# Kernel optimization log

Measured on AMD Instinct MI355X. Metric: run time of the kernel, lower is better.

## Reference

```python
import jax, jax.numpy as jnp
import numpy as np

N_EMBD = 512
Q_N_EMBD = 512
N_HEAD = 8
EPS = 1e-5


def _layernorm(x, w, b):
    mu = jnp.mean(x, axis=-1, keepdims=True)
    var = jnp.mean(jnp.square(x - mu), axis=-1, keepdims=True)
    return (x - mu) * jax.lax.rsqrt(var + EPS) * w + b


def setup_inputs() -> dict:
    key = jax.random.key(0)
    ks = jax.random.split(key, 16)
    B, C, H, W = 8, N_EMBD, 32, 32
    s = 1.0 / np.sqrt(N_EMBD)
    inp = {
        "q": jax.random.normal(ks[0], (B, Q_N_EMBD, H, W), jnp.float32),
        "kv": jax.random.normal(ks[1], (B, C, H, W), jnp.float32),
        "ln_kv_w": jnp.ones((N_EMBD,), jnp.float32),
        "ln_kv_b": jnp.zeros((N_EMBD,), jnp.float32),
        "ln_q_w": jnp.ones((Q_N_EMBD,), jnp.float32),
        "ln_q_b": jnp.zeros((Q_N_EMBD,), jnp.float32),
        "Wk": jax.random.normal(ks[2], (N_EMBD, N_EMBD), jnp.float32) * s,
        "bk": jnp.zeros((N_EMBD,), jnp.float32),
        "Wq": jax.random.normal(ks[3], (Q_N_EMBD, N_EMBD), jnp.float32) * s,
        "bq": jnp.zeros((N_EMBD,), jnp.float32),
        "Wv": jax.random.normal(ks[4], (N_EMBD, N_EMBD), jnp.float32) * s,
        "bv": jnp.zeros((N_EMBD,), jnp.float32),
        "Wp": jax.random.normal(ks[5], (N_EMBD, N_EMBD), jnp.float32) * s,
        "bp": jnp.zeros((N_EMBD,), jnp.float32),
    }
    return inp


def reference(q, kv, ln_kv_w, ln_kv_b, ln_q_w, ln_q_b,
              Wk, bk, Wq, bq, Wv, bv, Wp, bp):
    B, C, H, W = kv.shape
    c_q = q.shape[1]
    T = H * W
    hd = C // N_HEAD  # head dim

    # [B, C, H, W] -> [B, T, C] tokens
    kv_t = kv.reshape(B, C, T).transpose(0, 2, 1)
    q_t = q.reshape(B, c_q, T).transpose(0, 2, 1)

    kv_n = _layernorm(kv_t, ln_kv_w, ln_kv_b)
    q_n = _layernorm(q_t, ln_q_w, ln_q_b)

    # projections, split heads: [B, T, C] -> [B, H, T, hd]
    def heads(x):
        return x.reshape(B, T, N_HEAD, hd).transpose(0, 2, 1, 3)

    k = heads(kv_n @ Wk + bk)
    qh = heads(q_n @ Wq + bq)
    v = heads(kv_n @ Wv + bv)

    att = jnp.einsum('bhqd,bhkd->bhqk', qh, k) * (1.0 / np.sqrt(hd))
    att = jax.nn.softmax(att, axis=-1)
    y = jnp.einsum('bhqk,bhkd->bhqd', att, v)
    y = y.transpose(0, 2, 1, 3).reshape(B, T, C)
    y = y @ Wp + bp

    x = kv_t + y  # residual on (pre-LN) kv tokens
    return x.transpose(0, 2, 1).reshape(B, C, H, W)
```

## Files before the change

### kernel.cpp

```cpp
#include <hip/hip_runtime.h>
#include <stdint.h>

#define DI static __device__ __forceinline__

typedef __attribute__((ext_vector_type(8))) short bh8;
typedef __attribute__((ext_vector_type(4))) float f4;
typedef __attribute__((ext_vector_type(4))) unsigned int u4;

DI short f2bf(float f) {
  unsigned u = __float_as_uint(f);
  u += 0x7fffu + ((u >> 16) & 1u);
  return (short)(u >> 16);
}

DI unsigned pkbf(float a, float b) {
  unsigned ua = __float_as_uint(a) + 0x8000u;
  unsigned ub = __float_as_uint(b) + 0x8000u;
  return __builtin_amdgcn_perm(ub, ua, 0x07060302u);
}

DI void gll16(const void* g, void* l) {
  __builtin_amdgcn_global_load_lds(
      (const __attribute__((address_space(1))) unsigned int*)g,
      (__attribute__((address_space(3))) unsigned int*)l, 16, 0, 0);
}

DI f4 mfma16(bh8 a, bh8 b, f4 c) {
  return __builtin_amdgcn_mfma_f32_16x16x32_bf16(a, b, c, 0, 0, 0);
}

DI bh8 ld8(const short* p) { return *(const bh8*)p; }

__global__ __launch_bounds__(256) void prep_k(
    const float* __restrict__ kv, const float* __restrict__ qi,
    const float* __restrict__ kw, const float* __restrict__ kbv,
    const float* __restrict__ qw, const float* __restrict__ qbv,
    const float* __restrict__ Wk, const float* __restrict__ Wq,
    const float* __restrict__ Wv, const float* __restrict__ Wp,
    short* __restrict__ kvn, short* __restrict__ qn,
    short* __restrict__ Wt)
{
  __shared__ char sm[16 * 516 * 4 + 128];
  int role = blockIdx.y;
  int bx = blockIdx.x;
  int tid = threadIdx.x;

  if (role < 4) {
    if (bx >= 256) return;
    float (*ts)[33] = (float(*)[33])sm;
    const float* w = (role == 0) ? Wk : (role == 1) ? Wq : (role == 2) ? Wv : Wp;
    short* o = Wt + ((size_t)role << 18);
    int c0 = (bx & 15) << 5, r0 = (bx >> 4) << 5;
    int tx = tid & 31, ty = tid >> 5;
#pragma unroll
    for (int k = 0; k < 32; k += 8)
      ts[ty + k][tx] = w[((size_t)(r0 + ty + k) << 9) + c0 + tx];
    __syncthreads();
#pragma unroll
    for (int k = 0; k < 32; k += 8)
      o[((size_t)(c0 + ty + k) << 9) + r0 + tx] = f2bf(ts[tx][ty + k]);
    return;
  }

  float (*xs)[516] = (float(*)[516])sm;
  float* smean = (float*)(sm + 16 * 516 * 4);
  float* srstd = smean + 16;
  int which = role - 4;
  const float* x = which ? qi : kv;
  const float* w = which ? qw : kw;
  const float* bb = which ? qbv : kbv;
  short* o = which ? qn : kvn;
  int b = bx >> 6;
  int t0 = (bx & 63) << 4;
  const float* xb = x + ((size_t)b << 19) + (size_t)t0;
#pragma unroll
  for (int k = 0; k < 8; k++) {
    int idx = (k << 8) + tid;
    int c = idx >> 2, tt = (idx & 3) << 2;
    float4 v = *(const float4*)(xb + ((size_t)c << 10) + tt);
    xs[tt + 0][c] = v.x; xs[tt + 1][c] = v.y;
    xs[tt + 2][c] = v.z; xs[tt + 3][c] = v.w;
  }
  __syncthreads();
  {
    int t = tid >> 4, cp = tid & 15;
    float s = 0.f, s2 = 0.f;
#pragma unroll
    for (int k = 0; k < 8; k++) {
      float4 v = *(const float4*)&xs[t][(cp << 2) + (k << 6)];
      s  += v.x + v.y + v.z + v.w;
      s2 += v.x * v.x + v.y * v.y + v.z * v.z + v.w * v.w;
    }
#pragma unroll
    for (int m = 1; m < 16; m <<= 1) {
      s  += __shfl_xor(s,  m);
      s2 += __shfl_xor(s2, m);
    }
    if (cp == 0) {
      float mean = s * (1.f / 512.f);
      float var  = s2 * (1.f / 512.f) - mean * mean;
      smean[t] = mean;
      srstd[t] = rsqrtf(var + 1e-5f);
    }
  }
  __syncthreads();
#pragma unroll
  for (int k = 0; k < 8; k++) {
    int idx = (k << 8) + tid;
    int t = idx >> 7, c = (idx & 127) << 2;
    float4 v = *(const float4*)&xs[t][c];
    float4 wv = *(const float4*)(w + c);
    float4 bv4 = *(const float4*)(bb + c);
    float mu = smean[t], rs = srstd[t];
    float r0 = (v.x - mu) * rs * wv.x + bv4.x;
    float r1 = (v.y - mu) * rs * wv.y + bv4.y;
    float r2 = (v.z - mu) * rs * wv.z + bv4.z;
    float r3 = (v.w - mu) * rs * wv.w + bv4.w;
    uint2 pk; pk.x = pkbf(r0, r1); pk.y = pkbf(r2, r3);
    *(uint2*)(o + (((size_t)(b << 10) + t0 + t) << 9) + c) = pk;
  }
}

__global__ __launch_bounds__(256) void gemm_qkv_k(
    const short* __restrict__ kvn, const short* __restrict__ qn,
    const short* __restrict__ Wt,
    const float* __restrict__ bk, const float* __restrict__ bq,
    const float* __restrict__ bv,
    short* __restrict__ kbuf, short* __restrict__ qbuf,
    short* __restrict__ vtb)
{
  __shared__ short As[128 * 32];
  __shared__ short Bs[128 * 32];
  int z = blockIdx.z;
  const short* A; const short* Bt; const float* bias; short* outp;
  int m0, n0;
  if (z == 0)      { A = kvn;            Bt = Wt;             bias = bk; outp = kbuf; }
  else if (z == 1) { A = qn;             Bt = Wt + (1 << 18); bias = bq; outp = qbuf; }
  else             { A = Wt + (2 << 18); Bt = kvn;            bias = bv; outp = vtb; }
  if (z == 2) { m0 = blockIdx.y << 7; n0 = blockIdx.x << 7; }
  else        { m0 = blockIdx.x << 7; n0 = blockIdx.y << 7; }
  int tid = threadIdx.x;
  int lane = tid & 63, wid = tid >> 6;
  int r = lane & 15, g = lane >> 4;
  int wrow = (wid >> 1) << 6, wcol = (wid & 1) << 6;
  f4 acc[4][4];
#pragma unroll
  for (int i = 0; i < 4; i++)
#pragma unroll
    for (int j = 0; j < 4; j++) {
      acc[i][j][0] = 0.f; acc[i][j][1] = 0.f;
      acc[i][j][2] = 0.f; acc[i][j][3] = 0.f;
    }
  const short* Ag = A  + ((size_t)(m0 + (tid >> 2)) << 9) + ((tid & 3) << 3);
  const short* Bg = Bt + ((size_t)(n0 + (tid >> 2)) << 9) + ((tid & 3) << 3);
  short* Asl = As + tid * 8;
  short* Bsl = Bs + tid * 8;
  for (int k0 = 0; k0 < 512; k0 += 32) {
    __syncthreads();
    gll16(Ag + k0,            Asl);
    gll16(Ag + k0 + 64 * 512, Asl + 2048);
    gll16(Bg + k0,            Bsl);
    gll16(Bg + k0 + 64 * 512, Bsl + 2048);
    __syncthreads();
    bh8 a[4], b[4];
#pragma unroll
    for (int i = 0; i < 4; i++)
      a[i] = ld8(As + ((wrow + (i << 4) + r) << 5) + (g << 3));
#pragma unroll
    for (int j = 0; j < 4; j++)
      b[j] = ld8(Bs + ((wcol + (j << 4) + r) << 5) + (g << 3));
#pragma unroll
    for (int i = 0; i < 4; i++)
#pragma unroll
      for (int j = 0; j < 4; j++)
        acc[i][j] = mfma16(a[i], b[j], acc[i][j]);
  }
#pragma unroll
  for (int i = 0; i < 4; i++) {
#pragma unroll
    for (int j = 0; j < 4; j++) {
      int mm = m0 + wrow + (i << 4) + (g << 2);
      int nn = n0 + wcol + (j << 4) + r;
      if (z != 2) {
        float bvv = bias[nn];
        int h = nn >> 6, d = nn & 63;
#pragma unroll
        for (int q = 0; q < 4; q++) {
          int m = mm + q;
          int bb = m >> 10, t = m & 1023;
          outp[((((size_t)(bb * 8 + h)) << 10) + t) * 64 + d] =
              f2bf(acc[i][j][q] + bvv);
        }
      } else {
        int bb = nn >> 10, t = nn & 1023;
#pragma unroll
        for (int q = 0; q < 4; q++) {
          int m = mm + q;
          int h = m >> 6, d = m & 63;
          outp[((((size_t)(bb * 8 + h)) << 6) + d) * 1024 + t] =
              f2bf(acc[i][j][q] + bias[m]);
        }
      }
    }
  }
}

__global__ __launch_bounds__(256) void gemm_proj_k(
    const short* __restrict__ A, const short* __restrict__ Bt,
    const float* __restrict__ bias, float* __restrict__ outp,
    const float* __restrict__ resid)
{
  __shared__ short As[64 * 32];
  __shared__ short Bs[128 * 32];
  int m0 = blockIdx.y << 6, n0 = blockIdx.x << 7;
  int tid = threadIdx.x;
  int lane = tid & 63, wid = tid >> 6;
  int r = lane & 15, g = lane >> 4;
  int wrow = (wid >> 1) << 5, wcol = (wid & 1) << 6;
  f4 acc[2][4];
#pragma unroll
  for (int i = 0; i < 2; i++)
#pragma unroll
    for (int j = 0; j < 4; j++) {
      acc[i][j][0] = 0.f; acc[i][j][1] = 0.f;
      acc[i][j][2] = 0.f; acc[i][j][3] = 0.f;
    }
  const short* Ag = A  + ((size_t)(m0 + (tid >> 2)) << 9) + ((tid & 3) << 3);
  const short* Bg = Bt + ((size_t)(n0 + (tid >> 2)) << 9) + ((tid & 3) << 3);
  for (int k0 = 0; k0 < 512; k0 += 32) {
    __syncthreads();
    gll16(Ag + k0,            As + tid * 8);
    gll16(Bg + k0,            Bs + tid * 8);
    gll16(Bg + k0 + 64 * 512, Bs + 2048 + tid * 8);
    __syncthreads();
    bh8 a[2], b[4];
#pragma unroll
    for (int i = 0; i < 2; i++)
      a[i] = ld8(As + ((wrow + (i << 4) + r) << 5) + (g << 3));
#pragma unroll
    for (int j = 0; j < 4; j++)
      b[j] = ld8(Bs + ((wcol + (j << 4) + r) << 5) + (g << 3));
#pragma unroll
    for (int i = 0; i < 2; i++)
#pragma unroll
      for (int j = 0; j < 4; j++)
        acc[i][j] = mfma16(a[i], b[j], acc[i][j]);
  }
#pragma unroll
  for (int i = 0; i < 2; i++) {
#pragma unroll
    for (int j = 0; j < 4; j++) {
      int mm = m0 + wrow + (i << 4) + (g << 2);
      int nn = n0 + wcol + (j << 4) + r;
      int bb = nn >> 10, t = nn & 1023;
#pragma unroll
      for (int q = 0; q < 4; q++) {
        int m = mm + q;
        size_t ad = ((((size_t)bb << 9) + m) << 10) + t;
        outp[ad] = acc[i][j][q] + bias[m] + resid[ad];
      }
    }
  }
}

__global__ __launch_bounds__(256, 2) void attn_k(
    const short* __restrict__ qb, const short* __restrict__ kb,
    const short* __restrict__ vtb, short* __restrict__ yo)
{
  __shared__ short Ks[2 * 128 * 32];
  __shared__ short Vs[4 * 64 * 32];
  __shared__ short Ps[4 * 128 * 32];
  int h = blockIdx.x, b = blockIdx.z;
  int qt0 = blockIdx.y << 7;
  int tid = threadIdx.x, lane = tid & 63, wid = tid >> 6;
  int r = lane & 15, g = lane >> 4;
  int wbase = wid << 5;
  size_t bh = (size_t)(b * 8 + h);
  const short* Qg = qb  + ((bh << 10) + qt0) * 64;
  const short* Kg = kb  + (bh << 10) * 64;
  const short* Vg = vtb + (bh << 6) * 1024;

  bh8 qf[2][2];
#pragma unroll
  for (int i = 0; i < 2; i++)
#pragma unroll
    for (int ksd = 0; ksd < 2; ksd++)
      qf[i][ksd] = ld8(Qg + ((size_t)(wbase + (i << 4) + r) << 6) +
                       (ksd << 5) + (g << 3));

  bh8 ones;
#pragma unroll
  for (int j = 0; j < 8; j++) ones[j] = (short)0x3F80;

  f4 oac[2][4], sacc[2];
#pragma unroll
  for (int i = 0; i < 2; i++) {
#pragma unroll
    for (int jn = 0; jn < 4; jn++) {
      oac[i][jn][0] = 0.f; oac[i][jn][1] = 0.f;
      oac[i][jn][2] = 0.f; oac[i][jn][3] = 0.f;
    }
    sacc[i][0] = 0.f; sacc[i][1] = 0.f; sacc[i][2] = 0.f; sacc[i][3] = 0.f;
  }

  const float csc = 0.18033688011112042f;
  int u = (tid & 3) << 3;

  for (int ck = 0; ck < 8; ck++) {
    __syncthreads();
    {
      const short* Kc = Kg + ((size_t)ck << 13);
#pragma unroll
      for (int it = 0; it < 4; it++) {
        int c = ((it & 1) << 6) + (tid >> 2);
        int pc = ((c & 15) << 3) + (c >> 4);
        gll16(Kc + ((size_t)pc << 6) + ((it >> 1) << 5) + u,
              Ks + (it << 11) + (tid << 3));
      }
      const short* Vc = Vg + (ck << 7);
#pragma unroll
      for (int it = 0; it < 4; it++)
        gll16(Vc + ((size_t)(tid >> 2) << 10) + (it << 5) + u,
              Vs + (it << 11) + (tid << 3));
    }
    __syncthreads();

    f4 s[2][8];
#pragma unroll
    for (int i = 0; i < 2; i++)
#pragma unroll
      for (int j = 0; j < 8; j++) {
        s[i][j][0] = 0.f; s[i][j][1] = 0.f;
        s[i][j][2] = 0.f; s[i][j][3] = 0.f;
      }
#pragma unroll
    for (int ksd = 0; ksd < 2; ksd++)
#pragma unroll
      for (int j = 0; j < 8; j++) {
        bh8 bk8 = ld8(Ks + (ksd << 12) + (((j << 4) + r) << 5) + (g << 3));
#pragma unroll
        for (int i = 0; i < 2; i++)
          s[i][j] = mfma16(qf[i][ksd], bk8, s[i][j]);
      }

#pragma unroll
    for (int i = 0; i < 2; i++)
#pragma unroll
      for (int q = 0; q < 4; q++) {
        u4 pv;
        pv.x = pkbf(__builtin_amdgcn_exp2f(s[i][0][q] * csc),
                    __builtin_amdgcn_exp2f(s[i][1][q] * csc));
        pv.y = pkbf(__builtin_amdgcn_exp2f(s[i][2][q] * csc),
                    __builtin_amdgcn_exp2f(s[i][3][q] * csc));
        pv.z = pkbf(__builtin_amdgcn_exp2f(s[i][4][q] * csc),
                    __builtin_amdgcn_exp2f(s[i][5][q] * csc));
        pv.w = pkbf(__builtin_amdgcn_exp2f(s[i][6][q] * csc),
                    __builtin_amdgcn_exp2f(s[i][7][q] * csc));
        int row = wbase + (i << 4) + (g << 2) + q;
        int ec = ((r & 3) ^ ((row >> 2) + (r >> 2))) & 3;
        *(u4*)(Ps + ((r >> 2) << 12) + (row << 5) + (ec << 3)) = pv;
      }

#pragma unroll
    for (int ks = 0; ks < 4; ks++) {
      bh8 ap[2];
#pragma unroll
      for (int i = 0; i < 2; i++) {
        int row = wbase + (i << 4) + r;
        int ec = (g ^ ((row >> 2) + ks)) & 3;
        ap[i] = ld8(Ps + (ks << 12) + (row << 5) + (ec << 3));
        sacc[i] = mfma16(ap[i], ones, sacc[i]);
      }
#pragma unroll
      for (int jn = 0; jn < 4; jn++) {
        bh8 bv8 = ld8(Vs + (ks << 11) + (((jn << 4) + r) << 5) + (g << 3));
#pragma unroll
        for (int i = 0; i < 2; i++)
          oac[i][jn] = mfma16(ap[i], bv8, oac[i][jn]);
      }
    }
  }

#pragma unroll
  for (int i = 0; i < 2; i++)
#pragma unroll
    for (int q = 0; q < 4; q++) {
      float inv = 1.f / sacc[i][q];
      int trow = qt0 + wbase + (i << 4) + (g << 2) + q;
      size_t base = (((size_t)(b << 10) + trow) << 9) + (h << 6);
#pragma unroll
      for (int jn = 0; jn < 4; jn++)
        yo[base + (jn << 4) + r] = f2bf(oac[i][jn][q] * inv);
    }
}

extern "C" void kernel_launch(void* const* d_in, const int* in_sizes, int n_in,
                              void* d_out, int out_size, void* d_ws, size_t ws_size,
                              hipStream_t stream)
{
  const float* q    = (const float*)d_in[0];
  const float* kv   = (const float*)d_in[1];
  const float* lnkw = (const float*)d_in[2];
  const float* lnkb = (const float*)d_in[3];
  const float* lnqw = (const float*)d_in[4];
  const float* lnqb = (const float*)d_in[5];
  const float* Wk   = (const float*)d_in[6];
  const float* bk   = (const float*)d_in[7];
  const float* Wq   = (const float*)d_in[8];
  const float* bq   = (const float*)d_in[9];
  const float* Wv   = (const float*)d_in[10];
  const float* bv   = (const float*)d_in[11];
  const float* Wp   = (const float*)d_in[12];
  const float* bp   = (const float*)d_in[13];

  char* ws = (char*)d_ws;
  const size_t SZ = (size_t)8192 * 512 * 2;
  short* buf0 = (short*)(ws);
  short* qn   = (short*)(ws + SZ);
  short* kbuf = (short*)(ws + 2 * SZ);
  short* qbuf = (short*)(ws + 3 * SZ);
  short* vtb  = (short*)(ws + 4 * SZ);
  short* Wt   = (short*)(ws + 5 * SZ);
  if (ws_size < 5 * SZ + 4 * 512 * 512 * 2) return;

  prep_k<<<dim3(512, 6), 256, 0, stream>>>(kv, q, lnkw, lnkb, lnqw, lnqb,
                                           Wk, Wq, Wv, Wp, buf0, qn, Wt);
  gemm_qkv_k<<<dim3(64, 4, 3), 256, 0, stream>>>(buf0, qn, Wt, bk, bq, bv,
                                                 kbuf, qbuf, vtb);
  attn_k<<<dim3(8, 8, 8), 256, 0, stream>>>(qbuf, kbuf, vtb, buf0);
  gemm_proj_k<<<dim3(64, 8), 256, 0, stream>>>(Wt + (3 << 18), buf0, bp,
                                               (float*)d_out, kv);
}
```

Measured before the change: 176.0 us.

## Double GEMM K-tile to 64 with XOR-swizzled LDS layout

The QKV and projection GEMM kernels now stage 64-wide K slices per iteration instead of 32, which halves the number of barrier pairs per tile. The LDS layout is XOR-swizzled on 16-byte chunks to avoid bank conflicts on the wider rows. Launch-bound occupancy hints are added. The cost is twice the LDS per block and more live registers for the doubled fragment arrays.

```diff
diff --git a/kernel.cpp b/kernel.cpp
--- a/kernel.cpp
+++ b/kernel.cpp
@@ -121,7 +121,7 @@
   }
 }
 
-__global__ __launch_bounds__(256) void gemm_qkv_k(
+__global__ __launch_bounds__(256, 3) void gemm_qkv_k(
     const short* __restrict__ kvn, const short* __restrict__ qn,
     const short* __restrict__ Wt,
     const float* __restrict__ bk, const float* __restrict__ bq,
@@ -129,8 +129,8 @@
     short* __restrict__ kbuf, short* __restrict__ qbuf,
     short* __restrict__ vtb)
 {
-  __shared__ short As[128 * 32];
-  __shared__ short Bs[128 * 32];
+  __shared__ short As[128 * 64];
+  __shared__ short Bs[128 * 64];
   int z = blockIdx.z;
   const short* A; const short* Bt; const float* bias; short* outp;
   int m0, n0;
@@ -151,29 +151,38 @@
       acc[i][j][0] = 0.f; acc[i][j][1] = 0.f;
       acc[i][j][2] = 0.f; acc[i][j][3] = 0.f;
     }
-  const short* Ag = A  + ((size_t)(m0 + (tid >> 2)) << 9) + ((tid & 3) << 3);
-  const short* Bg = Bt + ((size_t)(n0 + (tid >> 2)) << 9) + ((tid & 3) << 3);
-  short* Asl = As + tid * 8;
-  short* Bsl = Bs + tid * 8;
-  for (int k0 = 0; k0 < 512; k0 += 32) {
-    __syncthreads();
-    gll16(Ag + k0,            Asl);
-    gll16(Ag + k0 + 64 * 512, Asl + 2048);
-    gll16(Bg + k0,            Bsl);
-    gll16(Bg + k0 + 64 * 512, Bsl + 2048);
-    __syncthreads();
-    bh8 a[4], b[4];
-#pragma unroll
-    for (int i = 0; i < 4; i++)
-      a[i] = ld8(As + ((wrow + (i << 4) + r) << 5) + (g << 3));
-#pragma unroll
-    for (int j = 0; j < 4; j++)
-      b[j] = ld8(Bs + ((wcol + (j << 4) + r) << 5) + (g << 3));
-#pragma unroll
-    for (int i = 0; i < 4; i++)
-#pragma unroll
-      for (int j = 0; j < 4; j++)
-        acc[i][j] = mfma16(a[i], b[j], acc[i][j]);
+  for (int k0 = 0; k0 < 512; k0 += 64) {
+    __syncthreads();
+#pragma unroll
+    for (int it = 0; it < 4; it++) {
+      int n = (it << 8) + tid;
+      int row = n >> 3;
+      int c = (n & 7) ^ (row & 7);
+      gll16(A  + ((size_t)(m0 + row) << 9) + k0 + (c << 3), As + (n << 3));
+      gll16(Bt + ((size_t)(n0 + row) << 9) + k0 + (c << 3), Bs + (n << 3));
+    }
+    __syncthreads();
+    bh8 a[2][4], b[2][4];
+#pragma unroll
+    for (int ks = 0; ks < 2; ks++) {
+#pragma unroll
+      for (int i = 0; i < 4; i++) {
+        int R = wrow + (i << 4) + r;
+        a[ks][i] = ld8(As + (R << 6) + ((((ks << 2) + g) ^ (R & 7)) << 3));
+      }
+#pragma unroll
+      for (int j = 0; j < 4; j++) {
+        int R = wcol + (j << 4) + r;
+        b[ks][j] = ld8(Bs + (R << 6) + ((((ks << 2) + g) ^ (R & 7)) << 3));
+      }
+    }
+#pragma unroll
+    for (int ks = 0; ks < 2; ks++)
+#pragma unroll
+      for (int i = 0; i < 4; i++)
+#pragma unroll
+        for (int j = 0; j < 4; j++)
+          acc[i][j] = mfma16(a[ks][i], b[ks][j], acc[i][j]);
   }
 #pragma unroll
   for (int i = 0; i < 4; i++) {
@@ -205,13 +214,13 @@
   }
 }
 
-__global__ __launch_bounds__(256) void gemm_proj_k(
+__global__ __launch_bounds__(256, 2) void gemm_proj_k(
     const short* __restrict__ A, const short* __restrict__ Bt,
     const float* __restrict__ bias, float* __restrict__ outp,
     const float* __restrict__ resid)
 {
-  __shared__ short As[64 * 32];
-  __shared__ short Bs[128 * 32];
+  __shared__ short As[64 * 64];
+  __shared__ short Bs[128 * 64];
   int m0 = blockIdx.y << 6, n0 = blockIdx.x << 7;
   int tid = threadIdx.x;
   int lane = tid & 63, wid = tid >> 6;
@@ -225,26 +234,44 @@
       acc[i][j][0] = 0.f; acc[i][j][1] = 0.f;
       acc[i][j][2] = 0.f; acc[i][j][3] = 0.f;
     }
-  const short* Ag = A  + ((size_t)(m0 + (tid >> 2)) << 9) + ((tid & 3) << 3);
-  const short* Bg = Bt + ((size_t)(n0 + (tid >> 2)) << 9) + ((tid & 3) << 3);
-  for (int k0 = 0; k0 < 512; k0 += 32) {
-    __syncthreads();
-    gll16(Ag + k0,            As + tid * 8);
-    gll16(Bg + k0,            Bs + tid * 8);
-    gll16(Bg + k0 + 64 * 512, Bs + 2048 + tid * 8);
-    __syncthreads();
-    bh8 a[2], b[4];
-#pragma unroll
-    for (int i = 0; i < 2; i++)
-      a[i] = ld8(As + ((wrow + (i << 4) + r) << 5) + (g << 3));
-#pragma unroll
-    for (int j = 0; j < 4; j++)
-      b[j] = ld8(Bs + ((wcol + (j << 4) + r) << 5) + (g << 3));
-#pragma unroll
-    for (int i = 0; i < 2; i++)
-#pragma unroll
-      for (int j = 0; j < 4; j++)
-        acc[i][j] = mfma16(a[i], b[j], acc[i][j]);
+  for (int k0 = 0; k0 < 512; k0 += 64) {
+    __syncthreads();
+#pragma unroll
+    for (int it = 0; it < 2; it++) {
+      int n = (it << 8) + tid;
+      int row = n >> 3;
+      int c = (n & 7) ^ (row & 7);
+      gll16(A + ((size_t)(m0 + row) << 9) + k0 + (c << 3), As + (n << 3));
+    }
+#pragma unroll
+    for (int it = 0; it < 4; it++) {
+      int n = (it << 8) + tid;
+      int row = n >> 3;
+      int c = (n & 7) ^ (row & 7);
+      gll16(Bt + ((size_t)(n0 + row) << 9) + k0 + (c << 3), Bs + (n << 3));
+    }
+    __syncthreads();
+    bh8 a[2][2], b[2][4];
+#pragma unroll
+    for (int ks = 0; ks < 2; ks++) {
+#pragma unroll
+      for (int i = 0; i < 2; i++) {
+        int R = wrow + (i << 4) + r;
+        a[ks][i] = ld8(As + (R << 6) + ((((ks << 2) + g) ^ (R & 7)) << 3));
+      }
+#pragma unroll
+      for (int j = 0; j < 4; j++) {
+        int R = wcol + (j << 4) + r;
+        b[ks][j] = ld8(Bs + (R << 6) + ((((ks << 2) + g) ^ (R & 7)) << 3));
+      }
+    }
+#pragma unroll
+    for (int ks = 0; ks < 2; ks++)
+#pragma unroll
+      for (int i = 0; i < 2; i++)
+#pragma unroll
+        for (int j = 0; j < 4; j++)
+          acc[i][j] = mfma16(a[ks][i], b[ks][j], acc[i][j]);
   }
 #pragma unroll
   for (int i = 0; i < 2; i++) {
```

New measurement: 172.2 us. 1.02x faster.
